# Optimization experiments

Measured on AMD Instinct MI355X. Metric: run time of the kernel, lower is better.

Reference implementation:

```python
import jax, jax.numpy as jnp
import numpy as np

N, E = 32768, 262144
IN_C, OUT_C = 128, 128
N_GRAPHS = 64


def setup_inputs() -> dict:
    key = jax.random.key(0)
    ks = jax.random.split(key, 8)
    x = jax.random.normal(ks[0], (N, IN_C), dtype=jnp.float32)
    edge_index = jax.random.randint(ks[1], (2, E), 0, N, dtype=jnp.int32)
    batch = jnp.sort(jax.random.randint(ks[2], (N,), 0, N_GRAPHS, dtype=jnp.int32))
    rand = jax.random.uniform(ks[3], (E,), dtype=jnp.float32)  # replaces random.random() draws
    lim_t = 1.0 / np.sqrt(IN_C)
    W_t = jax.random.uniform(ks[4], (IN_C, OUT_C), jnp.float32, -lim_t, lim_t)
    b_t = jax.random.uniform(ks[5], (OUT_C,), jnp.float32, -lim_t, lim_t)
    lim_s = 1.0 / np.sqrt(OUT_C)
    W_s = jax.random.uniform(ks[6], (OUT_C, 1), jnp.float32, -lim_s, lim_s)
    b_s = jax.random.uniform(ks[7], (1,), jnp.float32, -lim_s, lim_s)
    return dict(x=x, edge_index=edge_index, batch=batch, rand=rand,
                W_t=W_t, b_t=b_t, W_s=W_s, b_s=b_s)


def _greedy_match(scores, src, dst, rand, n):
    """Sequential greedy edge matching over score-sorted edges.
    Returns (order, cid_sorted, n_merged): cid_sorted[i] is the cluster id
    assigned to sorted edge i, or -1 if rejected/skipped."""
    scores = jax.lax.stop_gradient(scores)  # indices are non-differentiable (torch uses .item())
    rand = jax.lax.stop_gradient(rand)
    order = jnp.argsort(-scores)
    s_o, d_o = src[order], dst[order]
    acc = rand[order] <= scores[order]  # torch: skip edge if r > edge_score

    def step(carry, inp):
        avail, nxt = carry
        s, t, a = inp
        ok = a & avail[s] & avail[t]
        cid = jnp.where(ok, nxt, -1)
        avail = avail.at[s].set(avail[s] & ~ok)
        avail = avail.at[t].set(avail[t] & ~ok)
        return (avail, nxt + ok.astype(jnp.int32)), cid

    (_, n_merged), cid_sorted = jax.lax.scan(
        step, (jnp.ones((n,), bool), jnp.int32(0)), (s_o, d_o, acc))
    return order, cid_sorted, n_merged


def reference(x, edge_index, batch, rand, W_t, b_t, W_s, b_s):
    n = x.shape[0]
    src, dst = edge_index[0], edge_index[1]
    # merge_edge_sum + transform (eval mode, dropout p=0)
    x_merged = (x[src] + x[dst]) @ W_t + b_t          # [E, OUT_C]
    x_self = (x + x) @ W_t + b_t                      # [N, OUT_C] (self-edge merge)
    e = jax.nn.sigmoid((x_merged @ W_s).reshape(-1) + b_s[0])  # [E] edge scores

    order, cid_sorted, n_merged = _greedy_match(e, src, dst, rand, n)
    ok = cid_sorted >= 0                              # accepted sorted edges
    s_o, d_o = src[order], dst[order]

    # node -> cluster assignment (sentinel index n is dropped)
    cluster = jnp.full((n,), -1, jnp.int32)
    cluster = cluster.at[jnp.where(ok, s_o, n)].set(cid_sorted, mode='drop')
    cluster = cluster.at[jnp.where(ok, d_o, n)].set(cid_sorted, mode='drop')
    remaining = cluster < 0
    rem_rank = jnp.cumsum(remaining.astype(jnp.int32)) - 1  # ascending node order, like set iteration
    cluster = jnp.where(remaining, n_merged + rem_rank, cluster)
    num_clusters = n_merged + remaining.sum().astype(jnp.int32)

    # pooled features, padded to [n, OUT_C]; rows [0, num_clusters) are valid
    mcid = jnp.where(ok, cid_sorted, n)
    new_x = jnp.zeros((n, x_merged.shape[1]), x.dtype)
    new_x = new_x.at[mcid].set(x_merged[order], mode='drop')
    new_x = new_x.at[jnp.where(remaining, cluster, n)].set(x_self, mode='drop')

    # per-cluster edge score (1.0 for unmerged singleton nodes)
    new_edge_score = jnp.ones((n,), e.dtype).at[mcid].set(e[order], mode='drop')

    # new batch vector: new_batch[cluster[v]] = batch[v]
    new_batch = jnp.zeros((n,), batch.dtype).at[cluster].set(batch)

    # remapped edges + coalesce/remove_self_loops expressed as a validity mask
    new_ei = cluster[edge_index]                      # [2, E]
    key = new_ei[0].astype(jnp.int64) * n + new_ei[1].astype(jnp.int64)
    perm = jnp.argsort(key)
    ksorted = key[perm]
    first = jnp.concatenate([jnp.array([True]), ksorted[1:] != ksorted[:-1]])
    unique = jnp.zeros((key.shape[0],), bool).at[perm].set(first)
    edge_valid = unique & (new_ei[0] != new_ei[1])

    return new_x, cluster, new_batch, new_edge_score, num_clusters, new_ei, edge_valid, e
```

## Files before the change

### kernel.cpp

```cpp
#include <hip/hip_runtime.h>
#include <stdint.h>

typedef unsigned int u32;
typedef unsigned long long u64;

#define NN 32768
#define NE 262144
#define NC 128

#define O0 0u
#define O1 4194304u
#define O2 4227072u
#define O3 4259840u
#define O4 4292608u
#define O5 4292609u
#define O6 4816897u
#define O7 5079041u

#define HCAP (1u<<19)
#define NFULL 8
#define CNT0 8
#define MCAP 16384
#define SCAP 32768
#define SNB 32
#define MAXK 0xFFFFFFFFFFFFFFFFull
#define PREFLAG (1ull<<62)

__global__ void ep_init(const float* Wt, const float* Ws, const float* bt, const float* bs,
                        double* u, double* c0, u32* counters,
                        u64* b0, u64* b1, u32* avail, int* cl,
                        u32* tkey, u32* tmin) {
    u32 i = blockIdx.x*blockDim.x + threadIdx.x;
    if (blockIdx.x == 0 && threadIdx.x < 128) {
        int r = threadIdx.x;
        double s = 0.0;
        for (int j = 0; j < NC; j++) s += (double)Wt[r*NC+j] * (double)Ws[j];
        u[r] = s;
        if (r == 0) {
            double c = 0.0;
            for (int j = 0; j < NC; j++) c += (double)bt[j] * (double)Ws[j];
            *c0 = c + (double)bs[0];
        }
    }
    if (i < 64) counters[i] = 0u;
    if (i < NN) { b0[i] = MAXK; b1[i] = MAXK; cl[i] = -1; }
    if (i < NN/32) avail[i] = 0xFFFFFFFFu;
    for (u32 j = i; j < HCAP; j += 131072u) { tkey[j] = 0xFFFFFFFFu; tmin[j] = 0xFFFFFFFFu; }
}

__global__ void ep_ynode(const float* x, const double* u, double* y) {
    int gid = blockIdx.x*blockDim.x + threadIdx.x;
    int v = gid >> 6, lane = threadIdx.x & 63;
    if (v >= NN) return;
    double t = (double)x[v*NC+lane]*u[lane] + (double)x[v*NC+lane+64]*u[lane+64];
    for (int off = 32; off; off >>= 1) t += __shfl_down(t, off, 64);
    if (lane == 0) y[v] = t;
}

__global__ void ep_escore(const int* src, const int* dst, const float* rnd, const double* y,
                          const double* c0, u64* fkey, u64* fdat, u32* counters, float* out) {
    int e = blockIdx.x*blockDim.x + threadIdx.x;
    if (e >= NE) return;
    int s = src[e], d = dst[e];
    double z = y[s] + y[d] + *c0;
    double sc = 1.0/(1.0 + exp(-z));
    out[O7 + e] = (float)sc;
    u64 b = (u64)__double_as_longlong(z);
    u64 ord = (b & 0x8000000000000000ull) ? ~b : (b | 0x8000000000000000ull);
    u64 P = ((~ord) & 0xFFFFFFFFFFFC0000ull) | (u64)(u32)e;
    if ((double)rnd[e] <= sc) {
        u32 p = atomicAdd(&counters[CNT0], 1u);
        fkey[p] = P;
        fdat[p] = ((u64)(u32)e << 30) | ((u64)(u32)s << 15) | (u64)(u32)d;
    }
}

__device__ __forceinline__ bool ep_bit(const u32* a, u32 v) { return (a[v>>5] >> (v&31)) & 1u; }

__global__ void ep_rA(const u64* fkey, const u64* fdat, const u32* cnt, u64* bt, const u32* avail) {
    u32 n = *cnt;
    for (u32 i = blockIdx.x*blockDim.x + threadIdx.x; i < n; i += 131072u) {
        u64 v = fdat[i];
        u32 s = (u32)((v>>15)&0x7FFF), d = (u32)(v&0x7FFF);
        if (ep_bit(avail, s) && ep_bit(avail, d)) {
            u64 P = fkey[i];
            atomicMin(&bt[s], P); atomicMin(&bt[d], P);
        }
    }
}

__global__ void ep_rB(const u64* fkey, const u64* fdat, const u32* cnt, u32* cntN,
                      u64* fkeyN, u64* fdatN, const u64* bt, u64* btN, u32* avail,
                      u64* mkey, u64* mpay, u32* counters) {
    u32 n = *cnt;
    for (u32 i = blockIdx.x*blockDim.x + threadIdx.x; i < n; i += 131072u) {
        u64 v = fdat[i];
        u32 s = (u32)((v>>15)&0x7FFF), d = (u32)(v&0x7FFF);
        if (!ep_bit(avail, s) || !ep_bit(avail, d)) continue;
        u64 P = fkey[i];
        if (bt[s] == P && bt[d] == P) {
            u32 slot = atomicAdd(&counters[2], 1u);
            mkey[slot] = P; mpay[slot] = v;
            atomicAnd(&avail[s>>5], ~(1u<<(s&31)));
            atomicAnd(&avail[d>>5], ~(1u<<(d&31)));
        } else {
            u32 p = atomicAdd(cntN, 1u);
            fkeyN[p] = P; fdatN[p] = v;
            btN[s] = MAXK; btN[d] = MAXK;
        }
    }
}

__global__ void ep_merge(const u64* mk, const u64* mp, const u64* fk, const u64* fd,
                         u32* counters, u64* ck, u64* cd2) {
    u32 i = blockIdx.x*blockDim.x + threadIdx.x;
    u32 nm0 = counters[2];
    u32 cr  = counters[CNT0+NFULL];
    if (i == 0) { u32 tot = nm0 + cr; counters[4] = tot > SCAP ? SCAP : tot; }
    u64 K = MAXK, D = 0;
    if (i < nm0) { K = mk[i]; D = mp[i] | PREFLAG; }
    else if (i < nm0 + cr && i < SCAP) { K = fk[i-nm0]; D = fd[i-nm0]; }
    ck[i] = K; cd2[i] = D;
}

__device__ __forceinline__ u64 ep_peers(u32 d, bool real) {
    u64 m = ~0ull;
    #pragma unroll
    for (int b = 0; b < 8; b++) {
        u64 bb = __ballot((d >> b) & 1u);
        m &= ((d >> b) & 1u) ? bb : ~bb;
    }
    return m & __ballot(real);
}

__global__ void ms_hist(const u64* key, u32* hist, int shift, const u32* counters) {
    __shared__ u32 h[256];
    int t = threadIdx.x;
    u32 total = counters[4];
    h[t] = 0; h[t+64] = 0; h[t+128] = 0; h[t+192] = 0;
    u32 blk = blockIdx.x;
    for (int j = 0; j < 16; j++) {
        u32 idx = blk*1024u + (u32)j*64u + (u32)t;
        bool real = idx < total;
        u64 k = real ? key[idx] : MAXK;
        u32 d = (u32)(k >> shift) & 255u;
        u64 m = ep_peers(d, real);
        if (real && t == (__ffsll((unsigned long long)m) - 1)) h[d] += (u32)__popcll(m);
    }
    hist[(u32)t*SNB + blk]       = h[t];
    hist[((u32)t+64)*SNB + blk]  = h[t+64];
    hist[((u32)t+128)*SNB + blk] = h[t+128];
    hist[((u32)t+192)*SNB + blk] = h[t+192];
}

__global__ void ms_scan(u32* hist) {
    int t = threadIdx.x;
    int per = 256*SNB/64;
    int base = t*per;
    u32 s = 0;
    for (int j = 0; j < per; j++) s += hist[base+j];
    u32 x = s;
    for (int off = 1; off < 64; off <<= 1) { u32 yv = __shfl_up(x, off, 64); if (t >= off) x += yv; }
    u32 run = x - s;
    for (int j = 0; j < per; j++) { u32 tmp = hist[base+j]; hist[base+j] = run; run += tmp; }
}

__global__ void ms_scat(const u64* ki, const u64* pi, u64* ko, u64* po,
                        const u32* hist, int shift, const u32* counters) {
    __shared__ u32 cnt[256];
    int t = threadIdx.x;
    u32 total = counters[4];
    cnt[t] = 0; cnt[t+64] = 0; cnt[t+128] = 0; cnt[t+192] = 0;
    u32 blk = blockIdx.x;
    for (int j = 0; j < 16; j++) {
        u32 idx = blk*1024u + (u32)j*64u + (u32)t;
        bool real = idx < total;
        u64 k = real ? ki[idx] : MAXK;
        u32 d = (u32)(k >> shift) & 255u;
        u64 m = ep_peers(d, real);
        if (real) {
            u32 rank = (u32)__popcll(m & (((u64)1 << t) - 1ull));
            int leader = __ffsll((unsigned long long)m) - 1;
            u32 base = 0;
            if (t == leader) { base = cnt[d]; cnt[d] = base + (u32)__popcll(m); }
            base = __shfl(base, leader, 64);
            u32 pos = hist[d*SNB + blk] + base + rank;
            ko[pos] = k;
            po[pos] = pi[idx];
        }
    }
}

__global__ void ep_csum(const u64* sd, const u32* counters, u32* mflag, u32* csums) {
    u32 i = blockIdx.x*1024 + threadIdx.x;
    u32 cnt = counters[4];
    u64 v = sd[i];
    bool pre = (i < cnt) && ((v & PREFLAG) != 0);
    bool cand = (i < cnt) && !pre;
    mflag[i] = pre ? 1u : 0u;
    int c = __syncthreads_count(cand ? 1 : 0);
    if (threadIdx.x == 0) csums[blockIdx.x] = (u32)c;
}

__global__ void ep_cscan(u32* csums, u32* counters, int which) {
    int t = threadIdx.x;
    u32 v = (t < SNB) ? csums[t] : 0u;
    u32 x = v;
    for (int off = 1; off < 64; off <<= 1) { u32 y = __shfl_up(x, off, 64); if (t >= off) x += y; }
    if (t < SNB) csums[t] = x - v;
    if (t == SNB-1) counters[which] = x;
}

__global__ void ep_cemit(const u64* sd, const u32* counters, const u32* csums, u32* candIdx) {
    __shared__ u32 w[16];
    int t = threadIdx.x;
    u32 i = blockIdx.x*1024 + t;
    u32 cnt = counters[4];
    u64 v = sd[i];
    bool pre = (i < cnt) && ((v & PREFLAG) != 0);
    u32 c = ((i < cnt) && !pre) ? 1u : 0u;
    u32 x = c;
    for (int off = 1; off < 64; off <<= 1) { u32 y = __shfl_up(x, off, 64); if ((t&63) >= off) x += y; }
    if ((t&63) == 63) w[t>>6] = x;
    __syncthreads();
    if (t < 16) {
        u32 ww = w[t];
        for (int off = 1; off < 16; off <<= 1) { u32 y = __shfl_up(ww, off, 16); if (t >= off) ww += y; }
        w[t] = ww;
    }
    __syncthreads();
    u32 excl = ((t>>6) ? w[(t>>6)-1] : 0u) + x - c;
    if (c) candIdx[csums[blockIdx.x] + excl] = i;
}

__global__ void __launch_bounds__(1024) ep_walk(const u64* sd, const u32* candIdx,
                                                u32* counters, const u32* availG,
                                                u32* mflag, u32* msums) {
    __shared__ u32 avail[1024];
    __shared__ u32 claim[16384];
    __shared__ u32 part[1024];
    __shared__ u32 segs[32];
    int t = threadIdx.x;
    avail[t] = availG[t];
    for (int j = t; j < 16384; j += 1024) claim[j] = 0xFFFFFFFFu;
    __syncthreads();
    u32 ncand = counters[5];
    u32 iterTag = 0x3FFFFFu;
    for (u32 base = 0; base < ncand; base += 1024) {
        u32 j = base + (u32)t;
        bool have = j < ncand;
        u32 i = 0, s = 0, d = 0;
        if (have) {
            i = candIdx[j];
            u64 v = sd[i];
            s = (u32)((v>>15)&0x7FFF); d = (u32)(v&0x7FFF);
        }
        u32 hs = s & 16383u, hd = d & 16383u;
        int st = 1;
        if (have && ((avail[s>>5]>>(s&31))&1u) && ((avail[d>>5]>>(d&31))&1u)) st = 0;
        for (int guard = 0; guard < 2048; guard++) {
            u32 tag = (iterTag << 10) | (u32)t;
            if (st == 0) { atomicMin(&claim[hs], tag); atomicMin(&claim[hd], tag); }
            __syncthreads();
            if (st == 0) {
                bool aok = ((avail[s>>5]>>(s&31))&1u) && ((avail[d>>5]>>(d&31))&1u);
                if (!aok) st = 1;
                else if (claim[hs] == tag && claim[hd] == tag) {
                    st = 2;
                    atomicAnd(&avail[s>>5], ~(1u<<(s&31)));
                    atomicAnd(&avail[d>>5], ~(1u<<(d&31)));
                    mflag[i] = 1u;
                }
            }
            iterTag--;
            if (__syncthreads_count(st == 0) == 0) break;
        }
    }
    __syncthreads();
    u32 p = 0; int b2 = t*32;
    for (int j = 0; j < 32; j++) p += mflag[b2+j];
    part[t] = p;
    __syncthreads();
    if (t < 32) { u32 sg = 0; for (int j = 0; j < 32; j++) sg += part[t*32+j]; segs[t] = sg; }
    __syncthreads();
    if (t == 0) { u32 a = 0; for (int g = 0; g < 32; g++) { msums[g] = a; a += segs[g]; } counters[2] = a; }
}

__global__ void ep_memit(const u64* sd, const u32* mflag, const u32* msums,
                         const int* batch, u64* Mlist, int* cl, float* out) {
    __shared__ u32 w[16];
    int t = threadIdx.x;
    u32 i = blockIdx.x*1024 + t;
    u32 m = mflag[i];
    u32 x = m;
    for (int off = 1; off < 64; off <<= 1) { u32 y = __shfl_up(x, off, 64); if ((t&63) >= off) x += y; }
    if ((t&63) == 63) w[t>>6] = x;
    __syncthreads();
    if (t < 16) {
        u32 ww = w[t];
        for (int off = 1; off < 16; off <<= 1) { u32 y = __shfl_up(ww, off, 16); if (t >= off) ww += y; }
        w[t] = ww;
    }
    __syncthreads();
    u32 excl = ((t>>6) ? w[(t>>6)-1] : 0u) + x - m;
    if (m) {
        u32 cid = msums[blockIdx.x] + excl;
        u64 v = sd[i] & ~PREFLAG;
        u32 e = (u32)(v>>30), s = (u32)((v>>15)&0x7FFF), d = (u32)(v&0x7FFF);
        Mlist[cid] = v;
        cl[s] = (int)cid; cl[d] = (int)cid;
        u32 mx = s > d ? s : d;
        out[O2 + cid] = (float)batch[mx];
        out[O3 + cid] = out[O7 + e];
    }
}

__global__ void ep_scanN(int* cl, u32* counters, u32* slist, float* out) {
    __shared__ u32 w[16];
    int t = threadIdx.x;
    int base = t*32;
    u32 s = 0;
    for (int j = 0; j < 32; j++) s += (cl[base+j] < 0) ? 1u : 0u;
    u32 x = s;
    for (int off = 1; off < 64; off <<= 1) { u32 y = __shfl_up(x, off, 64); if ((t&63) >= off) x += y; }
    if ((t&63) == 63) w[t>>6] = x;
    __syncthreads();
    if (t < 16) {
        u32 ww = w[t];
        for (int off = 1; off < 16; off <<= 1) { u32 y = __shfl_up(ww, off, 16); if (t >= off) ww += y; }
        w[t] = ww;
    }
    __syncthreads();
    u32 excl = ((t>>6) ? w[(t>>6)-1] : 0u) + x - s;
    u32 total = w[15];
    u32 nm = counters[2];
    if (t == 0) {
        counters[3] = nm + total;
        counters[6] = total;
        out[O4] = (float)(nm + total);
    }
    u32 run = nm + excl;
    for (int j = 0; j < 32; j++) {
        if (cl[base+j] < 0) {
            slist[run - nm] = (u32)(base + j);
            cl[base+j] = (int)(run++);
        }
    }
}

__global__ void ep_out_nodes(const int* cl, const int* batch, const u32* counters, float* out) {
    int v = blockIdx.x*blockDim.x + threadIdx.x;
    if (v >= NN) return;
    u32 nm = counters[2], ncl = counters[3];
    int c = cl[v];
    out[O1 + v] = (float)c;
    if (c >= (int)nm) out[O2 + c] = (float)batch[v];
    if (v >= (int)nm) out[O3 + v] = 1.0f;
    if (v >= (int)ncl) out[O2 + v] = 0.0f;
}

__global__ void ep_newx_m(const float* x, const float* Wt, const float* bt,
                          const u64* Mlist, const u32* counters, float* out) {
    __shared__ u64 ml[32];
    __shared__ float m[32][128];
    u32 nm = counters[2];
    u32 base = blockIdx.x * 32u;
    if (base >= nm) return;
    int t = threadIdx.x, lane = t & 63, wv = t >> 6;
    if (t < 32) { u32 r = base + (u32)t; ml[t] = (r < nm) ? Mlist[r] : 0ull; }
    __syncthreads();
    for (int i = t; i < 4096; i += 256) {
        int r = i >> 7, k = i & 127;
        u64 v = ml[r];
        u32 s = (u32)((v>>15)&0x7FFF), d = (u32)(v&0x7FFF);
        m[r][k] = x[s*NC+k] + x[d*NC+k];
    }
    __syncthreads();
    float a0[8], a1[8];
    #pragma unroll
    for (int r = 0; r < 8; r++) { a0[r] = bt[lane]; a1[r] = bt[lane+64]; }
    for (int k = 0; k < 128; k++) {
        float w0 = Wt[k*NC+lane], w1 = Wt[k*NC+lane+64];
        #pragma unroll
        for (int r = 0; r < 8; r++) { float mm = m[wv*8+r][k]; a0[r] += mm*w0; a1[r] += mm*w1; }
    }
    #pragma unroll
    for (int r = 0; r < 8; r++) {
        u32 row = base + (u32)(wv*8 + r);
        if (row < nm) {
            out[O0 + (size_t)row*NC + lane]      = a0[r];
            out[O0 + (size_t)row*NC + lane + 64] = a1[r];
        }
    }
}

__global__ void ep_newx_s(const float* x, const float* Wt, const float* bt,
                          const u32* slist, const u32* counters, float* out) {
    __shared__ u32 nodes[32];
    __shared__ float m[32][128];
    u32 nm = counters[2], ncl = counters[3], sc = counters[6];
    u32 base = nm + blockIdx.x * 32u;
    if (base >= NN) return;
    int t = threadIdx.x, lane = t & 63, wv = t >> 6;
    if (base >= ncl) {
        for (int i = t; i < 4096; i += 256) {
            u32 row = base + (u32)(i >> 7);
            if (row < NN) out[O0 + (size_t)row*NC + (i & 127)] = 0.0f;
        }
        return;
    }
    if (t < 32) { u32 p = base - nm + (u32)t; nodes[t] = (p < sc) ? slist[p] : slist[0]; }
    __syncthreads();
    for (int i = t; i < 4096; i += 256) {
        int r = i >> 7, k = i & 127;
        m[r][k] = 2.0f * x[nodes[r]*NC + k];
    }
    __syncthreads();
    float a0[8], a1[8];
    #pragma unroll
    for (int r = 0; r < 8; r++) { a0[r] = bt[lane]; a1[r] = bt[lane+64]; }
    for (int k = 0; k < 128; k++) {
        float w0 = Wt[k*NC+lane], w1 = Wt[k*NC+lane+64];
        #pragma unroll
        for (int r = 0; r < 8; r++) { float mm = m[wv*8+r][k]; a0[r] += mm*w0; a1[r] += mm*w1; }
    }
    #pragma unroll
    for (int r = 0; r < 8; r++) {
        u32 row = base + (u32)(wv*8 + r);
        if (row >= NN) continue;
        if (row < ncl) {
            out[O0 + (size_t)row*NC + lane]      = a0[r];
            out[O0 + (size_t)row*NC + lane + 64] = a1[r];
        } else {
            out[O0 + (size_t)row*NC + lane]      = 0.0f;
            out[O0 + (size_t)row*NC + lane + 64] = 0.0f;
        }
    }
}

__global__ void ep_newei(const int* src, const int* dst, const int* cl,
                         u32* tkey, u32* tmin, u32* eslot, float* out) {
    int e = blockIdx.x*blockDim.x + threadIdx.x;
    if (e >= NE) return;
    u32 cs = (u32)cl[src[e]], cd = (u32)cl[dst[e]];
    out[O5 + e]      = (float)cs;
    out[O5 + NE + e] = (float)cd;
    u32 key = (cs << 15) | cd;
    u32 slot = ((key * 2654435761u) >> 11) & (HCAP-1);
    while (true) {
        u32 k = tkey[slot];
        if (k == key) break;
        if (k == 0xFFFFFFFFu) {
            u32 old = atomicCAS(&tkey[slot], 0xFFFFFFFFu, key);
            if (old == 0xFFFFFFFFu || old == key) break;
        }
        slot = (slot + 1) & (HCAP-1);
    }
    eslot[e] = slot | ((cs != cd) ? 0x80000000u : 0u);
    atomicMin(&tmin[slot], (u32)e);
}

__global__ void ep_valid(const u32* tmin, const u32* eslot, float* out) {
    int e = blockIdx.x*blockDim.x + threadIdx.x;
    if (e >= NE) return;
    u32 sl = eslot[e];
    bool valid = (tmin[sl & 0x7FFFFFFFu] == (u32)e) && (sl >> 31);
    out[O6 + e] = valid ? 1.0f : 0.0f;
}

extern "C" void kernel_launch(void* const* d_in, const int* in_sizes, int n_in,
                              void* d_out, int out_size, void* d_ws, size_t ws_size,
                              hipStream_t stream) {
    (void)in_sizes; (void)n_in; (void)out_size; (void)ws_size;
    const float* x    = (const float*)d_in[0];
    const int*   ei   = (const int*)d_in[1];
    const int*   src  = ei;
    const int*   dst  = ei + NE;
    const int*   batch= (const int*)d_in[2];
    const float* rnd  = (const float*)d_in[3];
    const float* Wt   = (const float*)d_in[4];
    const float* bt   = (const float*)d_in[5];
    const float* Ws   = (const float*)d_in[6];
    const float* bs   = (const float*)d_in[7];
    float* out = (float*)d_out;

    char* w = (char*)d_ws;
    double* u  = (double*)w;
    double* c0 = (double*)(w + 1024);
    u32* counters = (u32*)(w + 2048);
    size_t off = 4096;
    double* y   = (double*)(w + off); off += (size_t)NN*8;
    u64* fkeyA  = (u64*)(w + off); off += (size_t)NE*8;
    u64* fdatA  = (u64*)(w + off); off += (size_t)NE*8;
    u64* fkeyB  = (u64*)(w + off); off += (size_t)NE*8;
    u64* fdatB  = (u64*)(w + off); off += (size_t)NE*8;
    u64* mkeyA  = (u64*)(w + off); off += (size_t)MCAP*8;
    u64* mpayA  = (u64*)(w + off); off += (size_t)MCAP*8;
    u64* combK  = (u64*)(w + off); off += (size_t)SCAP*8;
    u64* combD  = (u64*)(w + off); off += (size_t)SCAP*8;
    u64* combK2 = (u64*)(w + off); off += (size_t)SCAP*8;
    u64* combD2 = (u64*)(w + off); off += (size_t)SCAP*8;
    u64* bt0    = (u64*)(w + off); off += (size_t)NN*8;
    u64* bt1    = (u64*)(w + off); off += (size_t)NN*8;
    u32* avail  = (u32*)(w + off); off += NN/8;
    int* cl     = (int*)(w + off); off += (size_t)NN*4;
    u64* Mlist  = (u64*)(w + off); off += (size_t)NN*8;
    u32* hist   = (u32*)(w + off); off += 8192*4;
    u32* mflag  = (u32*)(w + off); off += (size_t)SCAP*4;
    u32* candIdx= (u32*)(w + off); off += (size_t)SCAP*4;
    u32* csums  = (u32*)(w + off); off += 64*4;
    u32* msums  = (u32*)(w + off); off += 64*4;
    u32* slist  = (u32*)(w + off); off += (size_t)NN*4;
    u32* tkey   = (u32*)(w + off); off += (size_t)HCAP*4;
    u32* tmin   = (u32*)(w + off); off += (size_t)HCAP*4;
    u32* eslot  = (u32*)(w + off); off += (size_t)NE*4;

    ep_init<<<512, 256, 0, stream>>>(Wt, Ws, bt, bs, u, c0, counters,
                                     bt0, bt1, avail, cl, tkey, tmin);
    ep_ynode<<<8192, 256, 0, stream>>>(x, u, y);
    ep_escore<<<1024, 256, 0, stream>>>(src, dst, rnd, y, c0, fkeyA, fdatA, counters, out);

    u64 *fk = fkeyA, *fd = fdatA, *fk2 = fkeyB, *fd2 = fdatB;
    u64 *bc = bt0, *bn = bt1;
    for (u32 rd = 0; rd < NFULL; rd++) {
        ep_rA<<<512, 256, 0, stream>>>(fk, fd, &counters[CNT0+rd], bc, avail);
        ep_rB<<<512, 256, 0, stream>>>(fk, fd, &counters[CNT0+rd], &counters[CNT0+rd+1],
                                       fk2, fd2, bc, bn, avail, mkeyA, mpayA, counters);
        u64* tp;
        tp = fk; fk = fk2; fk2 = tp;
        tp = fd; fd = fd2; fd2 = tp;
        tp = bc; bc = bn; bn = tp;
    }

    ep_merge<<<SNB, 1024, 0, stream>>>(mkeyA, mpayA, fk, fd, counters, combK, combD);
    u64 *ki = combK, *pi = combD, *ko = combK2, *po = combD2;
    for (int p = 0; p < 6; p++) {
        int shift = 16 + p*8;
        ms_hist<<<SNB, 64, 0, stream>>>(ki, hist, shift, counters);
        ms_scan<<<1, 64, 0, stream>>>(hist);
        ms_scat<<<SNB, 64, 0, stream>>>(ki, pi, ko, po, hist, shift, counters);
        u64* tp;
        tp = ki; ki = ko; ko = tp;
        tp = pi; pi = po; po = tp;
    }

    ep_csum<<<SNB, 1024, 0, stream>>>(combD, counters, mflag, csums);
    ep_cscan<<<1, 64, 0, stream>>>(csums, counters, 5);
    ep_cemit<<<SNB, 1024, 0, stream>>>(combD, counters, csums, candIdx);
    ep_walk<<<1, 1024, 0, stream>>>(combD, candIdx, counters, avail, mflag, msums);
    ep_memit<<<SNB, 1024, 0, stream>>>(combD, mflag, msums, batch, Mlist, cl, out);

    ep_scanN<<<1, 1024, 0, stream>>>(cl, counters, slist, out);
    ep_out_nodes<<<128, 256, 0, stream>>>(cl, batch, counters, out);

    ep_newx_m<<<512, 256, 0, stream>>>(x, Wt, bt, Mlist, counters, out);
    ep_newx_s<<<1024, 256, 0, stream>>>(x, Wt, bt, slist, counters, out);

    ep_newei<<<1024, 256, 0, stream>>>(src, dst, cl, tkey, tmin, eslot, out);
    ep_valid<<<1024, 256, 0, stream>>>(tmin, eslot, out);
}
```

Before: 689.5 us.

## Drop payload arrays; recover edge endpoints from key's edge index

Removes the 64-bit payload arrays (fdat, mpay, combD) that traveled alongside sort keys through matching rounds and the radix sort. Endpoints are instead re-gathered from src/dst using the edge index in the key's low bits, and pre-matched status moves to a per-edge byte flag. This halves the sort's scatter traffic and the round traffic, at the cost of extra random gathers. It also retunes launch sizes: fewer round blocks, a 256-thread scan, and a 512-thread walk with a larger guard.

New measurement: 717.4 us. 1.04x slower.

```diff
diff --git a/kernel.cpp b/kernel.cpp
--- a/kernel.cpp
+++ b/kernel.cpp
@@ -24,12 +24,12 @@
 #define SCAP 32768
 #define SNB 32
 #define MAXK 0xFFFFFFFFFFFFFFFFull
-#define PREFLAG (1ull<<62)
+#define EMASK 0x3FFFFu
 
 __global__ void ep_init(const float* Wt, const float* Ws, const float* bt, const float* bs,
                         double* u, double* c0, u32* counters,
                         u64* b0, u64* b1, u32* avail, int* cl,
-                        u32* tkey, u32* tmin) {
+                        u32* tkey, u32* tmin, unsigned char* premat) {
     u32 i = blockIdx.x*blockDim.x + threadIdx.x;
     if (blockIdx.x == 0 && threadIdx.x < 128) {
         int r = threadIdx.x;
@@ -45,6 +45,7 @@
     if (i < 64) counters[i] = 0u;
     if (i < NN) { b0[i] = MAXK; b1[i] = MAXK; cl[i] = -1; }
     if (i < NN/32) avail[i] = 0xFFFFFFFFu;
+    ((unsigned short*)premat)[i] = 0;
     for (u32 j = i; j < HCAP; j += 131072u) { tkey[j] = 0xFFFFFFFFu; tmin[j] = 0xFFFFFFFFu; }
 }
 
@@ -58,7 +59,7 @@
 }
 
 __global__ void ep_escore(const int* src, const int* dst, const float* rnd, const double* y,
-                          const double* c0, u64* fkey, u64* fdat, u32* counters, float* out) {
+                          const double* c0, u64* fkey, u32* counters, float* out) {
     int e = blockIdx.x*blockDim.x + threadIdx.x;
     if (e >= NE) return;
     int s = src[e], d = dst[e];
@@ -71,56 +72,57 @@
     if ((double)rnd[e] <= sc) {
         u32 p = atomicAdd(&counters[CNT0], 1u);
         fkey[p] = P;
-        fdat[p] = ((u64)(u32)e << 30) | ((u64)(u32)s << 15) | (u64)(u32)d;
     }
 }
 
 __device__ __forceinline__ bool ep_bit(const u32* a, u32 v) { return (a[v>>5] >> (v&31)) & 1u; }
 
-__global__ void ep_rA(const u64* fkey, const u64* fdat, const u32* cnt, u64* bt, const u32* avail) {
+__global__ void ep_rA(const u64* fkey, const int* src, const int* dst,
+                      const u32* cnt, u64* bt, const u32* avail) {
     u32 n = *cnt;
-    for (u32 i = blockIdx.x*blockDim.x + threadIdx.x; i < n; i += 131072u) {
-        u64 v = fdat[i];
-        u32 s = (u32)((v>>15)&0x7FFF), d = (u32)(v&0x7FFF);
+    for (u32 i = blockIdx.x*blockDim.x + threadIdx.x; i < n; i += 65536u) {
+        u64 P = fkey[i];
+        u32 e = (u32)(P & EMASK);
+        u32 s = (u32)src[e], d = (u32)dst[e];
         if (ep_bit(avail, s) && ep_bit(avail, d)) {
-            u64 P = fkey[i];
             atomicMin(&bt[s], P); atomicMin(&bt[d], P);
         }
     }
 }
 
-__global__ void ep_rB(const u64* fkey, const u64* fdat, const u32* cnt, u32* cntN,
-                      u64* fkeyN, u64* fdatN, const u64* bt, u64* btN, u32* avail,
-                      u64* mkey, u64* mpay, u32* counters) {
+__global__ void ep_rB(const u64* fkey, const int* src, const int* dst,
+                      const u32* cnt, u32* cntN, u64* fkeyN,
+                      const u64* bt, u64* btN, u32* avail,
+                      u64* mkey, unsigned char* premat, u32* counters) {
     u32 n = *cnt;
-    for (u32 i = blockIdx.x*blockDim.x + threadIdx.x; i < n; i += 131072u) {
-        u64 v = fdat[i];
-        u32 s = (u32)((v>>15)&0x7FFF), d = (u32)(v&0x7FFF);
+    for (u32 i = blockIdx.x*blockDim.x + threadIdx.x; i < n; i += 65536u) {
+        u64 P = fkey[i];
+        u32 e = (u32)(P & EMASK);
+        u32 s = (u32)src[e], d = (u32)dst[e];
         if (!ep_bit(avail, s) || !ep_bit(avail, d)) continue;
-        u64 P = fkey[i];
         if (bt[s] == P && bt[d] == P) {
             u32 slot = atomicAdd(&counters[2], 1u);
-            mkey[slot] = P; mpay[slot] = v;
+            mkey[slot] = P;
+            premat[e] = 1;
             atomicAnd(&avail[s>>5], ~(1u<<(s&31)));
             atomicAnd(&avail[d>>5], ~(1u<<(d&31)));
         } else {
             u32 p = atomicAdd(cntN, 1u);
-            fkeyN[p] = P; fdatN[p] = v;
+            fkeyN[p] = P;
             btN[s] = MAXK; btN[d] = MAXK;
         }
     }
 }
 
-__global__ void ep_merge(const u64* mk, const u64* mp, const u64* fk, const u64* fd,
-                         u32* counters, u64* ck, u64* cd2) {
+__global__ void ep_merge(const u64* mk, const u64* fk, u32* counters, u64* ck) {
     u32 i = blockIdx.x*blockDim.x + threadIdx.x;
     u32 nm0 = counters[2];
     u32 cr  = counters[CNT0+NFULL];
     if (i == 0) { u32 tot = nm0 + cr; counters[4] = tot > SCAP ? SCAP : tot; }
-    u64 K = MAXK, D = 0;
-    if (i < nm0) { K = mk[i]; D = mp[i] | PREFLAG; }
-    else if (i < nm0 + cr && i < SCAP) { K = fk[i-nm0]; D = fd[i-nm0]; }
-    ck[i] = K; cd2[i] = D;
+    u64 K = MAXK;
+    if (i < nm0) K = mk[i];
+    else if (i < nm0 + cr && i < SCAP) K = fk[i-nm0];
+    ck[i] = K;
 }
 
 __device__ __forceinline__ u64 ep_peers(u32 d, bool real) {
@@ -154,19 +156,22 @@
 }
 
 __global__ void ms_scan(u32* hist) {
-    int t = threadIdx.x;
-    int per = 256*SNB/64;
-    int base = t*per;
+    __shared__ u32 w[4];
+    int t = threadIdx.x;
+    int base = t*32;
     u32 s = 0;
-    for (int j = 0; j < per; j++) s += hist[base+j];
+    for (int j = 0; j < 32; j++) s += hist[base+j];
     u32 x = s;
-    for (int off = 1; off < 64; off <<= 1) { u32 yv = __shfl_up(x, off, 64); if (t >= off) x += yv; }
-    u32 run = x - s;
-    for (int j = 0; j < per; j++) { u32 tmp = hist[base+j]; hist[base+j] = run; run += tmp; }
-}
-
-__global__ void ms_scat(const u64* ki, const u64* pi, u64* ko, u64* po,
-                        const u32* hist, int shift, const u32* counters) {
+    for (int off = 1; off < 64; off <<= 1) { u32 yv = __shfl_up(x, off, 64); if ((t&63) >= off) x += yv; }
+    if ((t&63) == 63) w[t>>6] = x;
+    __syncthreads();
+    if (t == 0) { u32 a = 0; for (int k = 0; k < 4; k++) { u32 tmp = w[k]; w[k] = a; a += tmp; } }
+    __syncthreads();
+    u32 run = w[t>>6] + x - s;
+    for (int j = 0; j < 32; j++) { u32 tmp = hist[base+j]; hist[base+j] = run; run += tmp; }
+}
+
+__global__ void ms_scat(const u64* ki, u64* ko, const u32* hist, int shift, const u32* counters) {
     __shared__ u32 cnt[256];
     int t = threadIdx.x;
     u32 total = counters[4];
@@ -184,18 +189,16 @@
             u32 base = 0;
             if (t == leader) { base = cnt[d]; cnt[d] = base + (u32)__popcll(m); }
             base = __shfl(base, leader, 64);
-            u32 pos = hist[d*SNB + blk] + base + rank;
-            ko[pos] = k;
-            po[pos] = pi[idx];
-        }
-    }
-}
-
-__global__ void ep_csum(const u64* sd, const u32* counters, u32* mflag, u32* csums) {
+            ko[hist[d*SNB + blk] + base + rank] = k;
+        }
+    }
+}
+
+__global__ void ep_csum(const u64* sk, const unsigned char* premat, const u32* counters,
+                        u32* mflag, u32* csums) {
     u32 i = blockIdx.x*1024 + threadIdx.x;
     u32 cnt = counters[4];
-    u64 v = sd[i];
-    bool pre = (i < cnt) && ((v & PREFLAG) != 0);
+    bool pre = (i < cnt) && premat[(u32)(sk[i] & EMASK)];
     bool cand = (i < cnt) && !pre;
     mflag[i] = pre ? 1u : 0u;
     int c = __syncthreads_count(cand ? 1 : 0);
@@ -211,13 +214,13 @@
     if (t == SNB-1) counters[which] = x;
 }
 
-__global__ void ep_cemit(const u64* sd, const u32* counters, const u32* csums, u32* candIdx) {
+__global__ void ep_cemit(const u64* sk, const unsigned char* premat, const u32* counters,
+                         const u32* csums, u32* candIdx) {
     __shared__ u32 w[16];
     int t = threadIdx.x;
     u32 i = blockIdx.x*1024 + t;
     u32 cnt = counters[4];
-    u64 v = sd[i];
-    bool pre = (i < cnt) && ((v & PREFLAG) != 0);
+    bool pre = (i < cnt) && premat[(u32)(sk[i] & EMASK)];
     u32 c = ((i < cnt) && !pre) ? 1u : 0u;
     u32 x = c;
     for (int off = 1; off < 64; off <<= 1) { u32 y = __shfl_up(x, off, 64); if ((t&63) >= off) x += y; }
@@ -233,32 +236,32 @@
     if (c) candIdx[csums[blockIdx.x] + excl] = i;
 }
 
-__global__ void __launch_bounds__(1024) ep_walk(const u64* sd, const u32* candIdx,
-                                                u32* counters, const u32* availG,
-                                                u32* mflag, u32* msums) {
+__global__ void __launch_bounds__(512) ep_walk(const u64* sk, const int* src, const int* dst,
+                                               const u32* candIdx, u32* counters,
+                                               const u32* availG, u32* mflag, u32* msums) {
     __shared__ u32 avail[1024];
     __shared__ u32 claim[16384];
-    __shared__ u32 part[1024];
+    __shared__ u32 part[512];
     __shared__ u32 segs[32];
     int t = threadIdx.x;
-    avail[t] = availG[t];
-    for (int j = t; j < 16384; j += 1024) claim[j] = 0xFFFFFFFFu;
+    avail[t] = availG[t]; avail[t+512] = availG[t+512];
+    for (int j = t; j < 16384; j += 512) claim[j] = 0xFFFFFFFFu;
     __syncthreads();
     u32 ncand = counters[5];
     u32 iterTag = 0x3FFFFFu;
-    for (u32 base = 0; base < ncand; base += 1024) {
+    for (u32 base = 0; base < ncand; base += 512) {
         u32 j = base + (u32)t;
         bool have = j < ncand;
         u32 i = 0, s = 0, d = 0;
         if (have) {
             i = candIdx[j];
-            u64 v = sd[i];
-            s = (u32)((v>>15)&0x7FFF); d = (u32)(v&0x7FFF);
+            u32 e = (u32)(sk[i] & EMASK);
+            s = (u32)src[e]; d = (u32)dst[e];
         }
         u32 hs = s & 16383u, hd = d & 16383u;
         int st = 1;
         if (have && ((avail[s>>5]>>(s&31))&1u) && ((avail[d>>5]>>(d&31))&1u)) st = 0;
-        for (int guard = 0; guard < 2048; guard++) {
+        for (int guard = 0; guard < 4096; guard++) {
             u32 tag = (iterTag << 10) | (u32)t;
             if (st == 0) { atomicMin(&claim[hs], tag); atomicMin(&claim[hd], tag); }
             __syncthreads();
@@ -277,16 +280,17 @@
         }
     }
     __syncthreads();
-    u32 p = 0; int b2 = t*32;
-    for (int j = 0; j < 32; j++) p += mflag[b2+j];
+    u32 p = 0; int b2 = t*64;
+    for (int j = 0; j < 64; j++) p += mflag[b2+j];
     part[t] = p;
     __syncthreads();
-    if (t < 32) { u32 sg = 0; for (int j = 0; j < 32; j++) sg += part[t*32+j]; segs[t] = sg; }
+    if (t < 32) { u32 sg = 0; for (int j = 0; j < 16; j++) sg += part[t*16+j]; segs[t] = sg; }
     __syncthreads();
     if (t == 0) { u32 a = 0; for (int g = 0; g < 32; g++) { msums[g] = a; a += segs[g]; } counters[2] = a; }
 }
 
-__global__ void ep_memit(const u64* sd, const u32* mflag, const u32* msums,
+__global__ void ep_memit(const u64* sk, const int* src, const int* dst,
+                         const u32* mflag, const u32* msums,
                          const int* batch, u64* Mlist, int* cl, float* out) {
     __shared__ u32 w[16];
     int t = threadIdx.x;
@@ -305,9 +309,9 @@
     u32 excl = ((t>>6) ? w[(t>>6)-1] : 0u) + x - m;
     if (m) {
         u32 cid = msums[blockIdx.x] + excl;
-        u64 v = sd[i] & ~PREFLAG;
-        u32 e = (u32)(v>>30), s = (u32)((v>>15)&0x7FFF), d = (u32)(v&0x7FFF);
-        Mlist[cid] = v;
+        u32 e = (u32)(sk[i] & EMASK);
+        u32 s = (u32)src[e], d = (u32)dst[e];
+        Mlist[cid] = ((u64)e << 30) | ((u64)s << 15) | (u64)d;
         cl[s] = (int)cid; cl[d] = (int)cid;
         u32 mx = s > d ? s : d;
         out[O2 + cid] = (float)batch[mx];
@@ -491,15 +495,10 @@
     size_t off = 4096;
     double* y   = (double*)(w + off); off += (size_t)NN*8;
     u64* fkeyA  = (u64*)(w + off); off += (size_t)NE*8;
-    u64* fdatA  = (u64*)(w + off); off += (size_t)NE*8;
     u64* fkeyB  = (u64*)(w + off); off += (size_t)NE*8;
-    u64* fdatB  = (u64*)(w + off); off += (size_t)NE*8;
     u64* mkeyA  = (u64*)(w + off); off += (size_t)MCAP*8;
-    u64* mpayA  = (u64*)(w + off); off += (size_t)MCAP*8;
     u64* combK  = (u64*)(w + off); off += (size_t)SCAP*8;
-    u64* combD  = (u64*)(w + off); off += (size_t)SCAP*8;
     u64* combK2 = (u64*)(w + off); off += (size_t)SCAP*8;
-    u64* combD2 = (u64*)(w + off); off += (size_t)SCAP*8;
     u64* bt0    = (u64*)(w + off); off += (size_t)NN*8;
     u64* bt1    = (u64*)(w + off); off += (size_t)NN*8;
     u32* avail  = (u32*)(w + off); off += NN/8;
@@ -511,44 +510,42 @@
     u32* csums  = (u32*)(w + off); off += 64*4;
     u32* msums  = (u32*)(w + off); off += 64*4;
     u32* slist  = (u32*)(w + off); off += (size_t)NN*4;
+    unsigned char* premat = (unsigned char*)(w + off); off += NE;
     u32* tkey   = (u32*)(w + off); off += (size_t)HCAP*4;
     u32* tmin   = (u32*)(w + off); off += (size_t)HCAP*4;
     u32* eslot  = (u32*)(w + off); off += (size_t)NE*4;
 
     ep_init<<<512, 256, 0, stream>>>(Wt, Ws, bt, bs, u, c0, counters,
-                                     bt0, bt1, avail, cl, tkey, tmin);
+                                     bt0, bt1, avail, cl, tkey, tmin, premat);
     ep_ynode<<<8192, 256, 0, stream>>>(x, u, y);
-    ep_escore<<<1024, 256, 0, stream>>>(src, dst, rnd, y, c0, fkeyA, fdatA, counters, out);
-
-    u64 *fk = fkeyA, *fd = fdatA, *fk2 = fkeyB, *fd2 = fdatB;
+    ep_escore<<<1024, 256, 0, stream>>>(src, dst, rnd, y, c0, fkeyA, counters, out);
+
+    u64 *fk = fkeyA, *fk2 = fkeyB;
     u64 *bc = bt0, *bn = bt1;
     for (u32 rd = 0; rd < NFULL; rd++) {
-        ep_rA<<<512, 256, 0, stream>>>(fk, fd, &counters[CNT0+rd], bc, avail);
-        ep_rB<<<512, 256, 0, stream>>>(fk, fd, &counters[CNT0+rd], &counters[CNT0+rd+1],
-                                       fk2, fd2, bc, bn, avail, mkeyA, mpayA, counters);
+        ep_rA<<<256, 256, 0, stream>>>(fk, src, dst, &counters[CNT0+rd], bc, avail);
+        ep_rB<<<256, 256, 0, stream>>>(fk, src, dst, &counters[CNT0+rd], &counters[CNT0+rd+1],
+                                       fk2, bc, bn, avail, mkeyA, premat, counters);
         u64* tp;
         tp = fk; fk = fk2; fk2 = tp;
-        tp = fd; fd = fd2; fd2 = tp;
         tp = bc; bc = bn; bn = tp;
     }
 
-    ep_merge<<<SNB, 1024, 0, stream>>>(mkeyA, mpayA, fk, fd, counters, combK, combD);
-    u64 *ki = combK, *pi = combD, *ko = combK2, *po = combD2;
+    ep_merge<<<SNB, 1024, 0, stream>>>(mkeyA, fk, counters, combK);
+    u64 *ki = combK, *ko = combK2;
     for (int p = 0; p < 6; p++) {
         int shift = 16 + p*8;
         ms_hist<<<SNB, 64, 0, stream>>>(ki, hist, shift, counters);
-        ms_scan<<<1, 64, 0, stream>>>(hist);
-        ms_scat<<<SNB, 64, 0, stream>>>(ki, pi, ko, po, hist, shift, counters);
-        u64* tp;
-        tp = ki; ki = ko; ko = tp;
-        tp = pi; pi = po; po = tp;
-    }
-
-    ep_csum<<<SNB, 1024, 0, stream>>>(combD, counters, mflag, csums);
+        ms_scan<<<1, 256, 0, stream>>>(hist);
+        ms_scat<<<SNB, 64, 0, stream>>>(ki, ko, hist, shift, counters);
+        u64* tp = ki; ki = ko; ko = tp;
+    }
+
+    ep_csum<<<SNB, 1024, 0, stream>>>(combK, premat, counters, mflag, csums);
     ep_cscan<<<1, 64, 0, stream>>>(csums, counters, 5);
-    ep_cemit<<<SNB, 1024, 0, stream>>>(combD, counters, csums, candIdx);
-    ep_walk<<<1, 1024, 0, stream>>>(combD, candIdx, counters, avail, mflag, msums);
-    ep_memit<<<SNB, 1024, 0, stream>>>(combD, mflag, msums, batch, Mlist, cl, out);
+    ep_cemit<<<SNB, 1024, 0, stream>>>(combK, premat, counters, csums, candIdx);
+    ep_walk<<<1, 512, 0, stream>>>(combK, src, dst, candIdx, counters, avail, mflag, msums);
+    ep_memit<<<SNB, 1024, 0, stream>>>(combK, src, dst, mflag, msums, batch, Mlist, cl, out);
 
     ep_scanN<<<1, 1024, 0, stream>>>(cl, counters, slist, out);
     ep_out_nodes<<<128, 256, 0, stream>>>(cl, batch, counters, out);
```
